# Optimization experiments

Hardware: AMD Instinct MI355X
Metric: run time of the kernel (lower is better)

The kernel has to match this reference:

```python
import jax, jax.numpy as jnp
import numpy as np

P = 7            # cfg.PATCH_SIZE_PHOTOMETRIC
BRIGHT = 0.02    # bright_threshold
BIG = 1e9        # masks invalid points out of kNN
K = 5            # neighbors for smoothness/slope


def _smooth_l1(x, y, beta):
    d = jnp.abs(x - y)
    return jnp.where(d < beta, 0.5 * d * d / beta, d - 0.5 * beta)


def _sample_patches(img, kp):
    # img: [B,1,H,W], kp: [B,N,2] (x,y) in pixel coords -> [B,1,N,P,P]
    # matches F.grid_sample(align_corners=True, bilinear, border): with the
    # module's normalization, sampling positions are exactly pixel coords.
    B, _, H, W = img.shape
    N = kp.shape[1]
    half = P // 2
    lin = jnp.linspace(-half, half, P)
    oy, ox = jnp.meshgrid(lin, lin, indexing='ij')  # patch index (i,j): +x=lin[j], +y=lin[i]
    px = jnp.clip(kp[..., 0:1] + ox.ravel(), 0.0, W - 1)  # [B,N,P*P]
    py = jnp.clip(kp[..., 1:2] + oy.ravel(), 0.0, H - 1)
    x0 = jnp.floor(px); y0 = jnp.floor(py)
    fx = px - x0; fy = py - y0
    x0i = jnp.clip(x0.astype(jnp.int32), 0, W - 1)
    x1i = jnp.clip(x0i + 1, 0, W - 1)
    y0i = jnp.clip(y0.astype(jnp.int32), 0, H - 1)
    y1i = jnp.clip(y0i + 1, 0, H - 1)
    im = img[:, 0]  # [B,H,W]
    b = jnp.arange(B)[:, None, None]
    v00 = im[b, y0i, x0i]; v01 = im[b, y0i, x1i]
    v10 = im[b, y1i, x0i]; v11 = im[b, y1i, x1i]
    val = (v00 * (1 - fx) + v01 * fx) * (1 - fy) + (v10 * (1 - fx) + v11 * fx) * fy
    return val.reshape(B, 1, N, P, P)


def _forward(lg, rg, kpl, kpr, scores, Q):
    B, N, _ = kpl.shape
    # ---- epipolar ----
    y_diff = jnp.abs(kpl[..., 1] - kpr[..., 1])
    ws = scores.sum()
    l_epipolar = jnp.where(ws > 1e-4, (y_diff * scores).sum() / jnp.maximum(ws, 1e-12), y_diff.mean())
    # ---- photometric + intensity ----
    pl = _sample_patches(lg, kpl)
    pr = _sample_patches(rg, kpr)
    c = P // 2
    center_l = pl[:, 0, :, c, c]  # [B,N]
    center_r = pr[:, 0, :, c, c]
    is_bright = (center_l > BRIGHT).astype(pl.dtype)
    diff = jnp.abs(pl - pr).mean(axis=(1, 3, 4))  # [B,N]
    w = scores * is_bright
    wsum = w.sum()
    safe = jnp.maximum(wsum, 1e-12)
    l_masked = jnp.where(wsum > 1e-4, (diff * w).sum() / safe, 0.0)
    l_intensity = jnp.where(wsum > 1e-4, (_smooth_l1(center_l, center_r, 1.0) * w).sum() / safe, 0.0)
    l_photo = l_masked + l_intensity
    # ---- disparity -> 3D ----
    disp = kpl[..., 0] - kpr[..., 0]
    pts4 = jnp.concatenate([kpl, disp[..., None], jnp.ones((B, N, 1), kpl.dtype)], axis=-1)
    proj = jnp.einsum('bni,bji->bnj', pts4, Q)
    Wc = jnp.maximum(proj[..., 3], 1e-6)
    p3d = proj[..., :3] / Wc[..., None]  # [B,N,3]
    Z = p3d[..., 2]
    valid = (Z > 100) & (Z < 30000) & (scores > 0.1)  # [B,N]
    # ---- kNN smoothness / slope / zero-mean (masked, vectorized) ----
    pm = p3d / 1000.0
    xy = pm[..., jnp.array([0, 2])]  # [B,N,2] horizontal plane
    h = pm[..., 1]                   # [B,N] height
    sq = (xy * xy).sum(-1)
    d2 = sq[:, :, None] + sq[:, None, :] - 2.0 * jnp.einsum('bnd,bmd->bnm', xy, xy)
    dist = jnp.sqrt(jnp.maximum(d2, 1e-12))  # [B,N,N]
    vm = valid[:, :, None] & valid[:, None, :]
    dist = jnp.where(vm, dist, BIG)
    negd, idx = jax.lax.top_k(-dist, K + 1)   # ascending distance
    nbr_idx = idx[:, :, 1:]                   # drop self
    nbr_d = jnp.maximum(-negd[:, :, 1:], 1e-3)
    b = jnp.arange(B)[:, None, None]
    nbr_h = h[b, nbr_idx]                     # [B,N,K]
    local_mean = nbr_h.mean(-1)
    n_valid = valid.sum(-1)
    nv = jnp.maximum(n_valid, 1).astype(h.dtype)
    vf = valid.astype(h.dtype)
    ls_b = (_smooth_l1(h, local_mean, 0.01) * vf).sum(-1) / nv
    slopes = jnp.abs(nbr_h - h[..., None]) / nbr_d
    pen = jax.nn.relu(slopes - 0.4)
    lsl_b = (pen * vf[..., None]).sum((-1, -2)) / (nv * K)
    lz_b = jnp.abs((h * vf).sum(-1) / nv)
    ok = (n_valid >= 10).astype(h.dtype)
    nb = jnp.maximum(ok.sum(), 1.0)
    gate = ((scores > 0.1).sum() >= 10) & (ok.sum() > 0)
    l_smooth = jnp.where(gate, (ls_b * ok).sum() / nb, 0.0)
    l_slope = jnp.where(gate, (lsl_b * ok).sum() / nb, 0.0)
    l_zeromean = jnp.where(gate, (lz_b * ok).sum() / nb, 0.0)
    return (l_photo, l_epipolar, l_smooth, l_slope, l_zeromean)


def setup_inputs() -> dict:
    key = jax.random.key(0)
    k = jax.random.split(key, 7)
    B, N, H, W = 16, 2000, 720, 1280
    lg = jax.random.uniform(k[0], (B, 1, H, W), dtype=jnp.float32)
    rg = jax.random.uniform(k[1], (B, 1, H, W), dtype=jnp.float32)
    kx = jax.random.uniform(k[2], (B, N), minval=200.0, maxval=1080.0)
    ky = jax.random.uniform(k[3], (B, N), minval=50.0, maxval=670.0)
    disp = jax.random.uniform(k[4], (B, N), minval=10.0, maxval=200.0)
    kpl = jnp.stack([kx, ky], -1)
    kpr = jnp.stack([kx - disp, ky + 0.5 * jax.random.normal(k[5], (B, N))], -1)
    scores = jax.random.uniform(k[6], (B, N), dtype=jnp.float32)
    f, cx, cy, Tx = 1000.0, 640.0, 360.0, 120.0  # focal px, principal point, baseline mm
    Qm = jnp.array([[1.0, 0.0, 0.0, -cx],
                    [0.0, 1.0, 0.0, -cy],
                    [0.0, 0.0, 0.0, f],
                    [0.0, 0.0, 1.0 / Tx, 0.0]], dtype=jnp.float32)
    Q = jnp.broadcast_to(Qm, (B, 4, 4))
    return {"lg": lg, "rg": rg, "kpl": kpl, "kpr": kpr, "scores": scores, "Q": Q}


def reference(lg, rg, kpl, kpr, scores, Q):
    return _forward(lg, rg, kpl, kpr, scores, Q)
```

## Files before the change

kernel.cpp:

```cpp
#include <hip/hip_runtime.h>

#define BB 16
#define NN 2000
#define HH 720
#define WW 1280
#define NPT (BB*NN)
#define PATCH_BLOCKS 1000
#define PROJ_BLOCKS (NPT/256)
#define KSTRIDE 2048
#define NS 4
#define SEGLEN (NN/NS)
#define SCAN_BLOCKS (8*NS*BB)
#define FUSED_BLOCKS 1536

static __device__ __forceinline__ unsigned u_min(unsigned a, unsigned b){ return a < b ? a : b; }

static __device__ __forceinline__ unsigned u_med3(unsigned a, unsigned b, unsigned c) {
    unsigned d;
    asm("v_med3_u32 %0, %1, %2, %3" : "=v"(d) : "v"(a), "v"(b), "v"(c));
    return d;
}

__device__ __forceinline__ void ins5(unsigned K[5], unsigned u) {
    K[4] = u_med3(K[3], K[4], u);
    K[3] = u_med3(K[2], K[3], u);
    K[2] = u_med3(K[1], K[2], u);
    K[1] = u_med3(K[0], K[1], u);
    K[0] = u_min(K[0], u);
}

__device__ __forceinline__ float bilin(const float* __restrict__ im, float px, float py) {
    px = fminf(fmaxf(px, 0.f), (float)(WW - 1));
    py = fminf(fmaxf(py, 0.f), (float)(HH - 1));
    float x0f = floorf(px), y0f = floorf(py);
    float fx = px - x0f, fy = py - y0f;
    int x0 = min(max((int)x0f, 0), WW - 1);
    int x1 = min(x0 + 1, WW - 1);
    int y0 = min(max((int)y0f, 0), HH - 1);
    int y1 = min(y0 + 1, HH - 1);
    const float* r0 = im + (size_t)y0 * WW;
    const float* r1 = im + (size_t)y1 * WW;
    float v00 = r0[x0], v01 = r0[x1], v10 = r1[x0], v11 = r1[x1];
    return (v00 * (1.f - fx) + v01 * fx) * (1.f - fy)
         + (v10 * (1.f - fx) + v11 * fx) * fy;
}

__global__ __launch_bounds__(256) void project_kernel(
    const float* __restrict__ kpl, const float* __restrict__ kpr,
    const float* __restrict__ scores, const float* __restrict__ Q,
    float4* __restrict__ pts, float* __restrict__ partialsA,
    float* __restrict__ batch_acc, unsigned* __restrict__ dcnt)
{
    if (blockIdx.x == 0) {
        if (threadIdx.x < BB * 4) batch_acc[threadIdx.x] = 0.f;
        if (threadIdx.x == BB * 4) *dcnt = 0u;
    }
    int pt = blockIdx.x * 256 + threadIdx.x;
    int b  = pt / NN;

    float2 kl = ((const float2* __restrict__)kpl)[pt];
    float2 kr = ((const float2* __restrict__)kpr)[pt];
    float sc  = scores[pt];
    float ydiff = fabsf(kl.y - kr.y);

    const float* q = Q + b * 16;
    float dsp = kl.x - kr.x;
    float p0 = q[0]*kl.x  + q[1]*kl.y  + q[2]*dsp  + q[3];
    float p1 = q[4]*kl.x  + q[5]*kl.y  + q[6]*dsp  + q[7];
    float p2 = q[8]*kl.x  + q[9]*kl.y  + q[10]*dsp + q[11];
    float p3 = q[12]*kl.x + q[13]*kl.y + q[14]*dsp + q[15];
    float Wc = fmaxf(p3, 1e-6f);
    float X = p0 / Wc, Y = p1 / Wc, Z = p2 / Wc;
    bool valid = (Z > 100.f) && (Z < 30000.f) && (sc > 0.1f);
    float x  = X / 1000.f;
    float hh = Y / 1000.f;
    float y  = Z / 1000.f;
    float sq = x * x + y * y;
    if (!valid) { x = 0.f; y = 0.f; sq = 1e18f; }
    pts[pt] = make_float4(x, y, sq, hh);

    float s0 = sc, s1 = ydiff * sc, s2 = ydiff, s3 = (sc > 0.1f) ? 1.f : 0.f;
    #pragma unroll
    for (int off = 32; off > 0; off >>= 1) {
        s0 += __shfl_down(s0, off, 64);
        s1 += __shfl_down(s1, off, 64);
        s2 += __shfl_down(s2, off, 64);
        s3 += __shfl_down(s3, off, 64);
    }
    __shared__ float red[4][4];
    int wave = threadIdx.x >> 6, lane = threadIdx.x & 63;
    if (lane == 0) { red[wave][0]=s0; red[wave][1]=s1; red[wave][2]=s2; red[wave][3]=s3; }
    __syncthreads();
    if (threadIdx.x < 4) {
        int k = threadIdx.x;
        partialsA[blockIdx.x * 4 + k] = red[0][k] + red[1][k] + red[2][k] + red[3][k];
    }
}

__global__ __launch_bounds__(256) void fused_patch_scan(
    const float* __restrict__ lg, const float* __restrict__ rg,
    const float* __restrict__ kpl, const float* __restrict__ kpr,
    const float* __restrict__ scores,
    const float4* __restrict__ pts, unsigned* __restrict__ keybuf,
    float* __restrict__ partialsB)
{
    int i = blockIdx.x;
    int m3 = i % 3;

    if (m3 != 2) {
        int pid = (i / 3) * 2 + m3;
        if (pid >= PATCH_BLOCKS) return;
        int wave = threadIdx.x >> 6, lane = threadIdx.x & 63;
        int rr = lane / 7, ci = lane - rr * 7;
        int s00 = lane + rr;
        if (s00 > 54) s00 = 54;
        int reg_r = lane >> 3, reg_c = lane & 7;

        float a3 = 0.f, a4l = 0.f, a5 = 0.f;

        for (int it = 0; it < 8; ++it) {
            int pt = pid * 32 + wave * 8 + it;
            int b = pt / NN;
            const float* iml = lg + (size_t)b * (HH * WW);
            const float* imr = rg + (size_t)b * (HH * WW);
            float kxl = kpl[2*pt], kyl = kpl[2*pt+1];
            float kxr = kpr[2*pt], kyr = kpr[2*pt+1];
            float sc  = scores[pt];

            float flx = floorf(kxl), fly = floorf(kyl);
            int xbl = (int)flx - 3, ybl = (int)fly - 3;
            float fxl = kxl - flx, fyl = kyl - fly;
            float vl = 0.f;
            if (xbl >= 0 && xbl <= WW-8 && ybl >= 0 && ybl <= HH-8) {
                float reg = iml[(size_t)(ybl + reg_r) * WW + xbl + reg_c];
                float v00 = __shfl(reg, s00,     64);
                float v01 = __shfl(reg, s00 + 1, 64);
                float v10 = __shfl(reg, s00 + 8, 64);
                float v11 = __shfl(reg, s00 + 9, 64);
                vl = (v00*(1.f-fxl) + v01*fxl)*(1.f-fyl) + (v10*(1.f-fxl) + v11*fxl)*fyl;
            } else if (lane < 49) {
                vl = bilin(iml, kxl + (float)(ci-3), kyl + (float)(rr-3));
            }
            float frx = floorf(kxr), fry = floorf(kyr);
            int xbr = (int)frx - 3, ybr = (int)fry - 3;
            float fxr = kxr - frx, fyr = kyr - fry;
            float vr = 0.f;
            if (xbr >= 0 && xbr <= WW-8 && ybr >= 0 && ybr <= HH-8) {
                float reg = imr[(size_t)(ybr + reg_r) * WW + xbr + reg_c];
                float v00 = __shfl(reg, s00,     64);
                float v01 = __shfl(reg, s00 + 1, 64);
                float v10 = __shfl(reg, s00 + 8, 64);
                float v11 = __shfl(reg, s00 + 9, 64);
                vr = (v00*(1.f-fxr) + v01*fxr)*(1.f-fyr) + (v10*(1.f-fxr) + v11*fxr)*fyr;
            } else if (lane < 49) {
                vr = bilin(imr, kxr + (float)(ci-3), kyr + (float)(rr-3));
            }

            float adiff = (lane < 49) ? fabsf(vl - vr) : 0.f;
            float cl = __shfl(vl, 24, 64);
            float cr = __shfl(vr, 24, 64);

            float isb = (cl > 0.02f) ? 1.f : 0.f;
            float w   = sc * isb;
            float dc  = fabsf(cl - cr);
            float sl1 = (dc < 1.f) ? 0.5f * dc * dc : dc - 0.5f;

            a3 += w;
            a5 += sl1 * w;
            a4l += w * adiff;
        }

        #pragma unroll
        for (int off = 32; off > 0; off >>= 1) a4l += __shfl_down(a4l, off, 64);

        __shared__ float red[4][3];
        if (lane == 0) { red[wave][0]=a3; red[wave][1]=a4l * (1.f/49.f); red[wave][2]=a5; }
        __syncthreads();
        if (threadIdx.x < 4) {
            int k = threadIdx.x;
            float v = 0.f;
            if (k < 3) v = red[0][k] + red[1][k] + red[2][k] + red[3][k];
            partialsB[pid * 4 + k] = v;
        }
    } else {
        __shared__ float4 seg[SEGLEN];
        int sid = i / 3;
        int bx   = sid & 7;
        int r    = sid >> 3;
        int segi = r & (NS - 1);
        int b    = r >> 2;
        int mseg0 = segi * SEGLEN;
        int n = bx * 256 + threadIdx.x;
        int nc = (n < NN) ? n : (NN - 1);

        const float4* cand = pts + b * NN + mseg0;
        for (int j = threadIdx.x; j < SEGLEN; j += 256) seg[j] = cand[j];

        float4 me = pts[b * NN + nc];
        float nx2 = -2.f * me.x, ny2 = -2.f * me.y, sqn = me.z;

        unsigned K[5] = {0xFFFFFFFFu,0xFFFFFFFFu,0xFFFFFFFFu,0xFFFFFFFFu,0xFFFFFFFFu};

        int nb0 = bx * 256;
        bool has_self = (mseg0 < nb0 + 256) && (mseg0 + SEGLEN > nb0);

        __syncthreads();

        if (has_self) {
            #pragma unroll 5
            for (int mm = 0; mm < SEGLEN; ++mm) {
                float4 o = seg[mm];
                int m = mseg0 + mm;
                float t = fmaf(ny2, o.y, o.z);
                t = fmaf(nx2, o.x, t);
                float d2 = fmaxf(t + sqn, 1e-12f);
                unsigned u = (__float_as_uint(d2) & 0xFFFFF800u) | (unsigned)m;
                u = (m == n) ? 0xFFFFFFFFu : u;
                ins5(K, u);
            }
        } else {
            #pragma unroll 5
            for (int mm = 0; mm < SEGLEN; ++mm) {
                float4 o = seg[mm];
                int m = mseg0 + mm;
                float t = fmaf(ny2, o.y, o.z);
                t = fmaf(nx2, o.x, t);
                float d2 = fmaxf(t + sqn, 1e-12f);
                unsigned u = (__float_as_uint(d2) & 0xFFFFF800u) | (unsigned)m;
                ins5(K, u);
            }
        }

        if (n < NN) {
            size_t base = (size_t)((b * NS + segi) * 5) * KSTRIDE + n;
            keybuf[base              ] = K[0];
            keybuf[base + KSTRIDE    ] = K[1];
            keybuf[base + KSTRIDE * 2] = K[2];
            keybuf[base + KSTRIDE * 3] = K[3];
            keybuf[base + KSTRIDE * 4] = K[4];
        }
    }
}

__global__ __launch_bounds__(256) void knn_merge_final(
    const float4* __restrict__ pts, const unsigned* __restrict__ keybuf,
    float* __restrict__ batch_acc, unsigned* __restrict__ dcnt,
    const float* __restrict__ partialsA, const float* __restrict__ partialsB,
    float* __restrict__ out)
{
    int b = blockIdx.y;
    int n = blockIdx.x * 256 + threadIdx.x;

    float ls = 0.f, pen = 0.f, hacc = 0.f, cnt = 0.f;
    if (n < NN) {
        float4 me = pts[b * NN + n];
        if (me.z < 1e17f) {
            unsigned K[5] = {0xFFFFFFFFu,0xFFFFFFFFu,0xFFFFFFFFu,0xFFFFFFFFu,0xFFFFFFFFu};
            #pragma unroll
            for (int s = 0; s < NS; ++s) {
                #pragma unroll
                for (int j = 0; j < 5; ++j) {
                    unsigned u = keybuf[(size_t)((b * NS + s) * 5 + j) * KSTRIDE + n];
                    ins5(K, u);
                }
            }
            float hsum = 0.f;
            #pragma unroll
            for (int t = 0; t < 5; ++t) {
                int idx = (int)(K[t] & 2047u);
                float4 o = pts[b * NN + idx];
                float dot = me.x * o.x + me.y * o.y;
                float d2 = (me.z + o.z) - 2.f * dot;
                float nd = fmaxf(sqrtf(fmaxf(d2, 1e-12f)), 0.001f);
                hsum += o.w;
                pen  += fmaxf(fabsf(o.w - me.w) / nd - 0.4f, 0.f);
            }
            float lm = hsum / 5.f;
            float dd = fabsf(me.w - lm);
            ls = (dd < 0.01f) ? 0.5f * dd * dd / 0.01f : dd - 0.005f;
            hacc = me.w;
            cnt  = 1.f;
        }
    }

    #pragma unroll
    for (int off = 32; off > 0; off >>= 1) {
        ls   += __shfl_down(ls,   off, 64);
        pen  += __shfl_down(pen,  off, 64);
        hacc += __shfl_down(hacc, off, 64);
        cnt  += __shfl_down(cnt,  off, 64);
    }
    __shared__ float r2[4][4];
    int wave = threadIdx.x >> 6, lane = threadIdx.x & 63;
    if (lane == 0) { r2[wave][0]=cnt; r2[wave][1]=ls; r2[wave][2]=pen; r2[wave][3]=hacc; }
    __syncthreads();
    if (threadIdx.x == 0) {
        float tc = r2[0][0]+r2[1][0]+r2[2][0]+r2[3][0];
        float tl = r2[0][1]+r2[1][1]+r2[2][1]+r2[3][1];
        float tp = r2[0][2]+r2[1][2]+r2[2][2]+r2[3][2];
        float th = r2[0][3]+r2[1][3]+r2[2][3]+r2[3][3];
        atomicAdd(&batch_acc[b * 4 + 0], tc);
        atomicAdd(&batch_acc[b * 4 + 1], tl);
        atomicAdd(&batch_acc[b * 4 + 2], tp);
        atomicAdd(&batch_acc[b * 4 + 3], th);
    }

    __shared__ int lastf;
    __threadfence();
    if (threadIdx.x == 0) {
        unsigned old = atomicAdd(dcnt, 1u);
        lastf = (old == (unsigned)(8 * BB - 1)) ? 1 : 0;
    }
    __syncthreads();
    if (!lastf) return;
    __threadfence();

    float s[7] = {0,0,0,0,0,0,0};
    for (int rI = threadIdx.x; rI < PROJ_BLOCKS; rI += 256) {
        s[0] += partialsA[rI * 4 + 0];
        s[1] += partialsA[rI * 4 + 1];
        s[2] += partialsA[rI * 4 + 2];
        s[3] += partialsA[rI * 4 + 3];
    }
    for (int rI = threadIdx.x; rI < PATCH_BLOCKS; rI += 256) {
        s[4] += partialsB[rI * 4 + 0];
        s[5] += partialsB[rI * 4 + 1];
        s[6] += partialsB[rI * 4 + 2];
    }
    #pragma unroll
    for (int off = 32; off > 0; off >>= 1) {
        #pragma unroll
        for (int k = 0; k < 7; ++k) s[k] += __shfl_down(s[k], off, 64);
    }
    __shared__ float ws2[4][7];
    if (lane == 0) {
        #pragma unroll
        for (int k = 0; k < 7; ++k) ws2[wave][k] = s[k];
    }
    __syncthreads();
    if (threadIdx.x == 0) {
        float t[7];
        #pragma unroll
        for (int k = 0; k < 7; ++k)
            t[k] = ws2[0][k] + ws2[1][k] + ws2[2][k] + ws2[3][k];
        float ssc = t[0], yds = t[1], yd = t[2], cnts = t[3];
        float wsum = t[4], dw = t[5], iw = t[6];

        float l_epi = (ssc > 1e-4f) ? yds / fmaxf(ssc, 1e-12f) : yd / (float)NPT;
        float safe = fmaxf(wsum, 1e-12f);
        float l_photo = (wsum > 1e-4f) ? (dw / safe + iw / safe) : 0.f;

        float als = 0.f, alsl = 0.f, alz = 0.f, okc = 0.f;
        for (int bb = 0; bb < BB; ++bb) {
            float nvf  = __hip_atomic_load(&batch_acc[bb*4+0], __ATOMIC_RELAXED, __HIP_MEMORY_SCOPE_AGENT);
            float lsb  = __hip_atomic_load(&batch_acc[bb*4+1], __ATOMIC_RELAXED, __HIP_MEMORY_SCOPE_AGENT);
            float penb = __hip_atomic_load(&batch_acc[bb*4+2], __ATOMIC_RELAXED, __HIP_MEMORY_SCOPE_AGENT);
            float hb   = __hip_atomic_load(&batch_acc[bb*4+3], __ATOMIC_RELAXED, __HIP_MEMORY_SCOPE_AGENT);
            float nv = fmaxf(nvf, 1.f);
            float ok = (nvf >= 10.f) ? 1.f : 0.f;
            als  += ok * (lsb / nv);
            alsl += ok * (penb / (nv * 5.f));
            alz  += ok * fabsf(hb / nv);
            okc  += ok;
        }
        float nb = fmaxf(okc, 1.f);
        bool gate = (cnts >= 10.f) && (okc > 0.f);
        out[0] = l_photo;
        out[1] = l_epi;
        out[2] = gate ? als / nb : 0.f;
        out[3] = gate ? alsl / nb : 0.f;
        out[4] = gate ? alz / nb : 0.f;
    }
}

extern "C" void kernel_launch(void* const* d_in, const int* in_sizes, int n_in,
                              void* d_out, int out_size, void* d_ws, size_t ws_size,
                              hipStream_t stream)
{
    const float* lg     = (const float*)d_in[0];
    const float* rg     = (const float*)d_in[1];
    const float* kpl    = (const float*)d_in[2];
    const float* kpr    = (const float*)d_in[3];
    const float* scores = (const float*)d_in[4];
    const float* Q      = (const float*)d_in[5];
    float* out = (float*)d_out;

    char* ws = (char*)d_ws;
    float4*   pts       = (float4*)ws;
    float*    partialsA = (float*)(ws + 512000);
    float*    partialsB = (float*)(ws + 514048);
    float*    batch_acc = (float*)(ws + 530432);
    unsigned* dcnt      = (unsigned*)(ws + 530688);
    unsigned* keybuf    = (unsigned*)(ws + 530944);

    project_kernel<<<PROJ_BLOCKS, 256, 0, stream>>>(kpl, kpr, scores, Q,
                                                    pts, partialsA, batch_acc, dcnt);
    fused_patch_scan<<<FUSED_BLOCKS, 256, 0, stream>>>(
        lg, rg, kpl, kpr, scores, pts, keybuf, partialsB);
    knn_merge_final<<<dim3(8, BB), 256, 0, stream>>>(pts, keybuf, batch_acc, dcnt,
                                                     partialsA, partialsB, out);
}
```

Baseline: 173.5 us.

## Fuse projection kernel into patch/scan kernel, recomputing projections locally in scan blocks

Merges the separate projection kernel into the fused patch/scan kernel by prepending projection blocks to the grid. The kNN scan blocks now recompute point projections directly from keypoints instead of reading pts, which removes the dependency on the earlier kernel. This drops one kernel launch and the inter-kernel serialization. The cost is redundant projection arithmetic, and the merge pass still reads pts written by the projection blocks.

Result: no change. 172.7 us (-0.4%).

```diff
diff --git a/kernel.cpp b/kernel.cpp
--- a/kernel.cpp
+++ b/kernel.cpp
@@ -10,8 +10,7 @@
 #define KSTRIDE 2048
 #define NS 4
 #define SEGLEN (NN/NS)
-#define SCAN_BLOCKS (8*NS*BB)
-#define FUSED_BLOCKS 1536
+#define FUSED_BLOCKS (PROJ_BLOCKS + 1536)
 
 static __device__ __forceinline__ unsigned u_min(unsigned a, unsigned b){ return a < b ? a : b; }
 
@@ -27,6 +26,24 @@
     K[2] = u_med3(K[1], K[2], u);
     K[1] = u_med3(K[0], K[1], u);
     K[0] = u_min(K[0], u);
+}
+
+__device__ __forceinline__ float4 project_pt(float2 kl, float2 kr, float sc,
+                                             const float* __restrict__ q) {
+    float dsp = kl.x - kr.x;
+    float p0 = q[0]*kl.x  + q[1]*kl.y  + q[2]*dsp  + q[3];
+    float p1 = q[4]*kl.x  + q[5]*kl.y  + q[6]*dsp  + q[7];
+    float p2 = q[8]*kl.x  + q[9]*kl.y  + q[10]*dsp + q[11];
+    float p3 = q[12]*kl.x + q[13]*kl.y + q[14]*dsp + q[15];
+    float Wc = fmaxf(p3, 1e-6f);
+    float X = p0 / Wc, Y = p1 / Wc, Z = p2 / Wc;
+    bool valid = (Z > 100.f) && (Z < 30000.f) && (sc > 0.1f);
+    float x  = X / 1000.f;
+    float hh = Y / 1000.f;
+    float y  = Z / 1000.f;
+    float sq = x * x + y * y;
+    if (!valid) { x = 0.f; y = 0.f; sq = 1e18f; }
+    return make_float4(x, y, sq, hh);
 }
 
 __device__ __forceinline__ float bilin(const float* __restrict__ im, float px, float py) {
@@ -45,70 +62,55 @@
          + (v10 * (1.f - fx) + v11 * fx) * fy;
 }
 
-__global__ __launch_bounds__(256) void project_kernel(
+__global__ __launch_bounds__(256) void fused_all(
+    const float* __restrict__ lg, const float* __restrict__ rg,
     const float* __restrict__ kpl, const float* __restrict__ kpr,
     const float* __restrict__ scores, const float* __restrict__ Q,
-    float4* __restrict__ pts, float* __restrict__ partialsA,
+    float4* __restrict__ pts, unsigned* __restrict__ keybuf,
+    float* __restrict__ partialsA, float* __restrict__ partialsB,
     float* __restrict__ batch_acc, unsigned* __restrict__ dcnt)
 {
-    if (blockIdx.x == 0) {
-        if (threadIdx.x < BB * 4) batch_acc[threadIdx.x] = 0.f;
-        if (threadIdx.x == BB * 4) *dcnt = 0u;
-    }
-    int pt = blockIdx.x * 256 + threadIdx.x;
-    int b  = pt / NN;
-
-    float2 kl = ((const float2* __restrict__)kpl)[pt];
-    float2 kr = ((const float2* __restrict__)kpr)[pt];
-    float sc  = scores[pt];
-    float ydiff = fabsf(kl.y - kr.y);
-
-    const float* q = Q + b * 16;
-    float dsp = kl.x - kr.x;
-    float p0 = q[0]*kl.x  + q[1]*kl.y  + q[2]*dsp  + q[3];
-    float p1 = q[4]*kl.x  + q[5]*kl.y  + q[6]*dsp  + q[7];
-    float p2 = q[8]*kl.x  + q[9]*kl.y  + q[10]*dsp + q[11];
-    float p3 = q[12]*kl.x + q[13]*kl.y + q[14]*dsp + q[15];
-    float Wc = fmaxf(p3, 1e-6f);
-    float X = p0 / Wc, Y = p1 / Wc, Z = p2 / Wc;
-    bool valid = (Z > 100.f) && (Z < 30000.f) && (sc > 0.1f);
-    float x  = X / 1000.f;
-    float hh = Y / 1000.f;
-    float y  = Z / 1000.f;
-    float sq = x * x + y * y;
-    if (!valid) { x = 0.f; y = 0.f; sq = 1e18f; }
-    pts[pt] = make_float4(x, y, sq, hh);
-
-    float s0 = sc, s1 = ydiff * sc, s2 = ydiff, s3 = (sc > 0.1f) ? 1.f : 0.f;
-    #pragma unroll
-    for (int off = 32; off > 0; off >>= 1) {
-        s0 += __shfl_down(s0, off, 64);
-        s1 += __shfl_down(s1, off, 64);
-        s2 += __shfl_down(s2, off, 64);
-        s3 += __shfl_down(s3, off, 64);
-    }
-    __shared__ float red[4][4];
-    int wave = threadIdx.x >> 6, lane = threadIdx.x & 63;
-    if (lane == 0) { red[wave][0]=s0; red[wave][1]=s1; red[wave][2]=s2; red[wave][3]=s3; }
-    __syncthreads();
-    if (threadIdx.x < 4) {
-        int k = threadIdx.x;
-        partialsA[blockIdx.x * 4 + k] = red[0][k] + red[1][k] + red[2][k] + red[3][k];
-    }
-}
-
-__global__ __launch_bounds__(256) void fused_patch_scan(
-    const float* __restrict__ lg, const float* __restrict__ rg,
-    const float* __restrict__ kpl, const float* __restrict__ kpr,
-    const float* __restrict__ scores,
-    const float4* __restrict__ pts, unsigned* __restrict__ keybuf,
-    float* __restrict__ partialsB)
-{
     int i = blockIdx.x;
-    int m3 = i % 3;
+
+    if (i < PROJ_BLOCKS) {
+        if (i == 0) {
+            if (threadIdx.x < BB * 4) batch_acc[threadIdx.x] = 0.f;
+            if (threadIdx.x == BB * 4) *dcnt = 0u;
+        }
+        int pt = i * 256 + threadIdx.x;
+        int b  = pt / NN;
+
+        float2 kl = ((const float2* __restrict__)kpl)[pt];
+        float2 kr = ((const float2* __restrict__)kpr)[pt];
+        float sc  = scores[pt];
+        float ydiff = fabsf(kl.y - kr.y);
+
+        pts[pt] = project_pt(kl, kr, sc, Q + b * 16);
+
+        float s0 = sc, s1 = ydiff * sc, s2 = ydiff, s3 = (sc > 0.1f) ? 1.f : 0.f;
+        #pragma unroll
+        for (int off = 32; off > 0; off >>= 1) {
+            s0 += __shfl_down(s0, off, 64);
+            s1 += __shfl_down(s1, off, 64);
+            s2 += __shfl_down(s2, off, 64);
+            s3 += __shfl_down(s3, off, 64);
+        }
+        __shared__ float redA[4][4];
+        int wave = threadIdx.x >> 6, lane = threadIdx.x & 63;
+        if (lane == 0) { redA[wave][0]=s0; redA[wave][1]=s1; redA[wave][2]=s2; redA[wave][3]=s3; }
+        __syncthreads();
+        if (threadIdx.x < 4) {
+            int k = threadIdx.x;
+            partialsA[i * 4 + k] = redA[0][k] + redA[1][k] + redA[2][k] + redA[3][k];
+        }
+        return;
+    }
+
+    int j = i - PROJ_BLOCKS;
+    int m3 = j % 3;
 
     if (m3 != 2) {
-        int pid = (i / 3) * 2 + m3;
+        int pid = (j / 3) * 2 + m3;
         if (pid >= PATCH_BLOCKS) return;
         int wave = threadIdx.x >> 6, lane = threadIdx.x & 63;
         int rr = lane / 7, ci = lane - rr * 7;
@@ -174,7 +176,8 @@
         for (int off = 32; off > 0; off >>= 1) a4l += __shfl_down(a4l, off, 64);
 
         __shared__ float red[4][3];
-        if (lane == 0) { red[wave][0]=a3; red[wave][1]=a4l * (1.f/49.f); red[wave][2]=a5; }
+        int wv = threadIdx.x >> 6;
+        if (lane == 0) { red[wv][0]=a3; red[wv][1]=a4l * (1.f/49.f); red[wv][2]=a5; }
         __syncthreads();
         if (threadIdx.x < 4) {
             int k = threadIdx.x;
@@ -184,19 +187,30 @@
         }
     } else {
         __shared__ float4 seg[SEGLEN];
-        int sid = i / 3;
+        int sid = j / 3;
         int bx   = sid & 7;
         int r    = sid >> 3;
         int segi = r & (NS - 1);
         int b    = r >> 2;
         int mseg0 = segi * SEGLEN;
+        const float* q = Q + b * 16;
+
+        for (int jj = threadIdx.x; jj < SEGLEN; jj += 256) {
+            int p = b * NN + mseg0 + jj;
+            float2 kl = ((const float2* __restrict__)kpl)[p];
+            float2 kr = ((const float2* __restrict__)kpr)[p];
+            seg[jj] = project_pt(kl, kr, scores[p], q);
+        }
+
         int n = bx * 256 + threadIdx.x;
         int nc = (n < NN) ? n : (NN - 1);
-
-        const float4* cand = pts + b * NN + mseg0;
-        for (int j = threadIdx.x; j < SEGLEN; j += 256) seg[j] = cand[j];
-
-        float4 me = pts[b * NN + nc];
+        float4 me;
+        {
+            int p = b * NN + nc;
+            float2 kl = ((const float2* __restrict__)kpl)[p];
+            float2 kr = ((const float2* __restrict__)kpr)[p];
+            me = project_pt(kl, kr, scores[p], q);
+        }
         float nx2 = -2.f * me.x, ny2 = -2.f * me.y, sqn = me.z;
 
         unsigned K[5] = {0xFFFFFFFFu,0xFFFFFFFFu,0xFFFFFFFFu,0xFFFFFFFFu,0xFFFFFFFFu};
@@ -259,8 +273,8 @@
             #pragma unroll
             for (int s = 0; s < NS; ++s) {
                 #pragma unroll
-                for (int j = 0; j < 5; ++j) {
-                    unsigned u = keybuf[(size_t)((b * NS + s) * 5 + j) * KSTRIDE + n];
+                for (int jj = 0; jj < 5; ++jj) {
+                    unsigned u = keybuf[(size_t)((b * NS + s) * 5 + jj) * KSTRIDE + n];
                     ins5(K, u);
                 }
             }
@@ -393,10 +407,9 @@
     unsigned* dcnt      = (unsigned*)(ws + 530688);
     unsigned* keybuf    = (unsigned*)(ws + 530944);
 
-    project_kernel<<<PROJ_BLOCKS, 256, 0, stream>>>(kpl, kpr, scores, Q,
-                                                    pts, partialsA, batch_acc, dcnt);
-    fused_patch_scan<<<FUSED_BLOCKS, 256, 0, stream>>>(
-        lg, rg, kpl, kpr, scores, pts, keybuf, partialsB);
+    fused_all<<<FUSED_BLOCKS, 256, 0, stream>>>(
+        lg, rg, kpl, kpr, scores, Q, pts, keybuf,
+        partialsA, partialsB, batch_acc, dcnt);
     knn_merge_final<<<dim3(8, BB), 256, 0, stream>>>(pts, keybuf, batch_acc, dcnt,
                                                      partialsA, partialsB, out);
 }
```
